# Kernel tuning notes

Hardware: AMD Instinct MI355X
Metric: run time of the kernel (lower is better)

The kernel has to match this reference:

```python
import jax, jax.numpy as jnp
import numpy as np

NC = 16       # class_nums
C = 128       # in_channel == EMBEND_DIM
NS = 8192     # support points
NQ = 30000    # query points
EPS = 1e-8


def setup_inputs() -> dict:
    key = jax.random.key(0)
    ks = jax.random.split(key, 7)
    support_features = jax.random.normal(ks[0], (NS, C), dtype=jnp.float32)
    support_labels = jax.random.randint(ks[1], (NS,), 0, NC)
    query_features = jax.random.normal(ks[2], (NQ, C), dtype=jnp.float32)
    # proj = Linear(2C+1 -> C) + ReLU + Linear(C -> 128)
    s1 = 1.0 / np.sqrt(2 * C + 1)
    W1 = jax.random.uniform(ks[3], (2 * C + 1, C), minval=-s1, maxval=s1, dtype=jnp.float32)
    b1 = jax.random.uniform(ks[4], (C,), minval=-s1, maxval=s1, dtype=jnp.float32)
    s2 = 1.0 / np.sqrt(C)
    W2 = jax.random.uniform(ks[5], (C, C), minval=-s2, maxval=s2, dtype=jnp.float32)
    b2 = jax.random.uniform(ks[6], (C,), minval=-s2, maxval=s2, dtype=jnp.float32)
    return {"support_features": support_features, "support_labels": support_labels,
            "query_features": query_features, "W1": W1, "b1": b1, "W2": W2, "b2": b2}


def _prototypes(support_features, support_labels):
    # fused scatter-mean replacing the per-class Python loop
    sums = jax.ops.segment_sum(support_features, support_labels, num_segments=NC)  # [Nc, C]
    counts = jax.ops.segment_sum(jnp.ones((support_features.shape[0],), support_features.dtype),
                                 support_labels, num_segments=NC)                   # [Nc]
    return jnp.where(counts[:, None] > 0, sums / jnp.maximum(counts, 1.0)[:, None], 0.0)


def reference(support_features, support_labels, query_features, W1, b1, W2, b2):
    protos = _prototypes(support_features, support_labels)                # [Nc, C]
    # MD_distance: cosine similarity between each query and each class prototype
    qn = query_features / jnp.maximum(jnp.linalg.norm(query_features, axis=-1, keepdims=True), EPS)
    pn = protos / jnp.maximum(jnp.linalg.norm(protos, axis=-1, keepdims=True), EPS)
    cos = jnp.einsum('qc,nc->qn', qn, pn)                                 # [Nq, Nc]
    # proj(cat([query, proto, cos], -1)) without materializing the [Nq,Nc,2C+1] concat:
    # split W1 rows into query part, proto part, and cos part.
    Wq, Wp, Wc = W1[:C], W1[C:2 * C], W1[2 * C]                           # [C,C],[C,C],[C]
    h = jax.nn.relu(jnp.einsum('qc,ch->qh', query_features, Wq)[:, None, :]
                    + jnp.einsum('nc,ch->nh', protos, Wp)[None, :, :]
                    + cos[:, :, None] * Wc[None, None, :]
                    + b1)                                                 # [Nq, Nc, C]
    similarity = jnp.einsum('qnh,ho->qno', h, W2) + b2                    # [Nq, Nc, 128]
    return similarity, cos[:, :, None]
```

## Files before the change

### kernel.cpp

```cpp
#include <hip/hip_runtime.h>

#define NQ_ 30000
#define NC_ 16
#define C_  128
#define NS_ 8192
#define QB  16
#define NBLK (NQ_/QB)

typedef __attribute__((ext_vector_type(4))) float  f32x4;
typedef __attribute__((ext_vector_type(4))) short  s16x4;
typedef __attribute__((ext_vector_type(8))) short  s16x8;

#define WS_PART  0
#define WS_PCNT  32768
#define WS_T     33024
#define WS_PACK  35072

__device__ inline short f2bf(float x){
  unsigned u = __float_as_uint(x);
  u += 0x7fffu + ((u >> 16) & 1u);
  return (short)(u >> 16);
}

__global__ __launch_bounds__(128) void protoA(const float* __restrict__ sf,
                                              const int* __restrict__ lbl,
                                              const float* __restrict__ W1,
                                              const float* __restrict__ W2,
                                              float* __restrict__ ws){
  const int b = blockIdx.x;
  const int t = threadIdx.x;
  if (b < 256){
    const int cls = b >> 4;
    const int ch  = b & 15;
    const int r0  = ch * (NS_/16);
    float s = 0.f; int cnt = 0;
    #pragma unroll 4
    for (int r = r0; r < r0 + NS_/16; ++r){
      if (lbl[r] == cls){ s += sf[(size_t)r*C_ + t]; ++cnt; }
    }
    ws[WS_PART + (cls*16 + ch)*C_ + t] = s;
    if (t == 0) ws[WS_PCNT + cls*16 + ch] = (float)cnt;
  } else {
    short* packo = (short*)(ws + WS_PACK);
    const int g0 = (b - 256)*1024 + t*8;
    const int gg = g0 & 16383;
    const int ln = (gg >> 3) & 63, ks = (gg >> 9) & 3, wvv = gg >> 11;
    const int kb = ks*32 + ((ln >> 4) & 3)*8;
    const int col = wvv*16 + (ln & 15);
    const float* src = (g0 < 16384) ? W2 : W1;
    s16x8 v;
    #pragma unroll
    for (int i = 0; i < 8; ++i) v[i] = f2bf(src[(size_t)(kb + i)*C_ + col]);
    *(s16x8*)&packo[g0] = v;
  }
}

__global__ __launch_bounds__(128) void protoB(const float* __restrict__ W1,
                                              const float* __restrict__ b1,
                                              float* __restrict__ ws){
  __shared__ float pr[C_];
  __shared__ float rns;
  const int n = blockIdx.x;
  const int h = threadIdx.x;
  float s = 0.f;
  #pragma unroll
  for (int ch = 0; ch < 16; ++ch) s += ws[WS_PART + (n*16 + ch)*C_ + h];
  float cnt = 0.f;
  #pragma unroll
  for (int ch = 0; ch < 16; ++ch) cnt += ws[WS_PCNT + n*16 + ch];
  const float pv = (cnt > 0.f) ? s / fmaxf(cnt, 1.f) : 0.f;
  pr[h] = pv;
  __syncthreads();
  if (h < 64){
    float q = pr[h]*pr[h] + pr[h+64]*pr[h+64];
    q += __shfl_xor(q, 1);  q += __shfl_xor(q, 2);  q += __shfl_xor(q, 4);
    q += __shfl_xor(q, 8);  q += __shfl_xor(q, 16); q += __shfl_xor(q, 32);
    if (h == 0) rns = 1.f / fmaxf(sqrtf(q), 1e-8f);
  }
  __syncthreads();
  {
    short* packo = (short*)(ws + WS_PACK);
    const int k = h;
    const int gg = ((k >> 5)*64 + ((k >> 3) & 3)*16 + n)*8 + (k & 7);
    packo[32768 + gg] = f2bf(pv * rns);
  }
  float acc = b1[h];
  #pragma unroll 8
  for (int c = 0; c < C_; ++c) acc = fmaf(pr[c], W1[(size_t)(C_ + c)*C_ + h], acc);
  ws[WS_T + n*C_ + h] = acc;
}

__global__ __launch_bounds__(512) void fused_main(const float* __restrict__ qfeat,
                                                  const float* __restrict__ W1,
                                                  const float* __restrict__ b2,
                                                  const float* __restrict__ ws,
                                                  float* __restrict__ out){
  __shared__ __align__(16) char un[16384];
  __shared__ float qw[QB][132];
  __shared__ float tl16[NC_][132];
  __shared__ float cosl[QB][NC_];
  __shared__ float rqn[QB];
  __shared__ float wcl[C_];

  float (*qfs)[132] = (float(*)[132])un;
  short* hfrag = (short*)un;

  const int t    = threadIdx.x;
  const int lane = t & 63;
  const int wv   = t >> 6;
  const int qbase = blockIdx.x * QB;
  float* out_cos = out + (size_t)NQ_ * NC_ * C_;
  const short* pack = (const short*)(ws + WS_PACK);

  {
    int idx = t * 4; int q = idx >> 7; int c = idx & 127;
    *(f32x4*)&qfs[q][c]  = *(const f32x4*)(qfeat + (size_t)qbase*C_ + idx);
    *(f32x4*)&tl16[q][c] = *(const f32x4*)(ws + WS_T + idx);
    if (t < 32) *(f32x4*)&wcl[t*4] = *(const f32x4*)(W1 + 2*C_*C_ + t*4);
  }
  __syncthreads();

  if (t < 128){
    int q = t >> 3; int c0 = (t & 7) * 16;
    float s = 0.f;
    #pragma unroll
    for (int m = 0; m < 16; ++m){ float v = qfs[q][c0+m]; s = fmaf(v, v, s); }
    s += __shfl_xor(s, 1); s += __shfl_xor(s, 2); s += __shfl_xor(s, 4);
    if ((t & 7) == 0) rqn[q] = 1.f / fmaxf(sqrtf(s), 1e-8f);
  }

  const int fr = lane & 15;
  const int fg = lane >> 4;
  const int ocol = wv*16 + fr;

  s16x8 qfr[4], w2f[4], wqf[4];
  #pragma unroll
  for (int ks = 0; ks < 4; ++ks){
    const int c0 = ks*32 + fg*8;
    f32x4 a = *(const f32x4*)&qfs[fr][c0];
    f32x4 b = *(const f32x4*)&qfs[fr][c0+4];
    s16x8 v;
    v[0]=f2bf(a[0]); v[1]=f2bf(a[1]); v[2]=f2bf(a[2]); v[3]=f2bf(a[3]);
    v[4]=f2bf(b[0]); v[5]=f2bf(b[1]); v[6]=f2bf(b[2]); v[7]=f2bf(b[3]);
    qfr[ks] = v;
    w2f[ks] = *(const s16x8*)&pack[((wv*4 + ks)*64 + lane)*8];
    wqf[ks] = *(const s16x8*)&pack[16384 + ((wv*4 + ks)*64 + lane)*8];
  }
  const float b2v = b2[ocol];
  __syncthreads();

  {
    f32x4 dq = {0.f,0.f,0.f,0.f};
    #pragma unroll
    for (int ks = 0; ks < 4; ++ks)
      dq = __builtin_amdgcn_mfma_f32_16x16x32_bf16(qfr[ks], wqf[ks], dq, 0,0,0);
    #pragma unroll
    for (int r = 0; r < 4; ++r) qw[fg*4 + r][ocol] = dq[r];
  }
  if (wv == 0){
    s16x8 pnf[4];
    #pragma unroll
    for (int ks = 0; ks < 4; ++ks)
      pnf[ks] = *(const s16x8*)&pack[32768 + (ks*64 + lane)*8];
    f32x4 dc = {0.f,0.f,0.f,0.f};
    #pragma unroll
    for (int ks = 0; ks < 4; ++ks)
      dc = __builtin_amdgcn_mfma_f32_16x16x32_bf16(qfr[ks], pnf[ks], dc, 0,0,0);
    #pragma unroll
    for (int r = 0; r < 4; ++r){
      const int q = fg*4 + r;
      const float cv = dc[r] * rqn[q];
      cosl[q][fr] = cv;
      out_cos[(size_t)(qbase + q)*NC_ + fr] = cv;
    }
  }
  __syncthreads();

  const int na  = lane & 15;
  const int ga  = lane >> 4;
  const int ksA = wv >> 1;
  const int ii0 = (wv & 1) * 4;
  const int k0  = ksA*32 + ga*8 + ii0;
  const f32x4 t4  = *(const f32x4*)&tl16[na][k0];
  const f32x4 wc4 = *(const f32x4*)&wcl[k0];

  #pragma unroll
  for (int chunk = 0; chunk < 4; ++chunk){
    const int q0 = chunk * 4;
    #pragma unroll
    for (int qq = 0; qq < 4; ++qq){
      const int q = q0 + qq;
      f32x4 qw4 = *(const f32x4*)&qw[q][k0];
      const float cv = cosl[q][na];
      s16x4 hv;
      #pragma unroll
      for (int j = 0; j < 4; ++j){
        float h = fmaf(cv, wc4[j], qw4[j] + t4[j]);
        hv[j] = f2bf(fmaxf(h, 0.f));
      }
      *(s16x4*)&hfrag[qq*2048 + ksA*512 + lane*8 + ii0] = hv;
    }
    __syncthreads();
    #pragma unroll
    for (int qq = 0; qq < 4; ++qq){
      s16x8 a0 = *(const s16x8*)&hfrag[qq*2048 +    0 + lane*8];
      s16x8 a1 = *(const s16x8*)&hfrag[qq*2048 +  512 + lane*8];
      s16x8 a2 = *(const s16x8*)&hfrag[qq*2048 + 1024 + lane*8];
      s16x8 a3 = *(const s16x8*)&hfrag[qq*2048 + 1536 + lane*8];
      f32x4 acc = {b2v, b2v, b2v, b2v};
      acc = __builtin_amdgcn_mfma_f32_16x16x32_bf16(a0, w2f[0], acc, 0,0,0);
      acc = __builtin_amdgcn_mfma_f32_16x16x32_bf16(a1, w2f[1], acc, 0,0,0);
      acc = __builtin_amdgcn_mfma_f32_16x16x32_bf16(a2, w2f[2], acc, 0,0,0);
      acc = __builtin_amdgcn_mfma_f32_16x16x32_bf16(a3, w2f[3], acc, 0,0,0);
      const size_t qout = (size_t)(qbase + q0 + qq) * (NC_*C_);
      #pragma unroll
      for (int r = 0; r < 4; ++r)
        out[qout + (fg*4 + r)*C_ + ocol] = acc[r];
    }
    __syncthreads();
  }
}

extern "C" void kernel_launch(void* const* d_in, const int* in_sizes, int n_in,
                              void* d_out, int out_size, void* d_ws, size_t ws_size,
                              hipStream_t stream){
  const float* sf  = (const float*)d_in[0];
  const int*   lbl = (const int*)  d_in[1];
  const float* qf  = (const float*)d_in[2];
  const float* W1  = (const float*)d_in[3];
  const float* b1  = (const float*)d_in[4];
  const float* W2  = (const float*)d_in[5];
  const float* b2  = (const float*)d_in[6];
  float* ws  = (float*)d_ws;
  float* out = (float*)d_out;

  protoA<<<288, 128, 0, stream>>>(sf, lbl, W1, W2, ws);
  protoB<<<NC_, 128, 0, stream>>>(W1, b1, ws);
  fused_main<<<NBLK, 512, 0, stream>>>(qf, W1, b2, ws, out);
}
```

Before: 89.38 us.

## Single-pass all-class prototype reduction and packed bf16 conversions

Prototype accumulation now has each of 64 chunks read the support rows once and accumulate into all 16 class registers. Before, 256 blocks each re-read a slice and filtered by a single class. Separately, float-to-bf16 conversions in the main kernel use the packed HIP bf16x2 intrinsic in place of manual per-element rounding. The first change cuts redundant support-feature reads and uses more registers per thread. The second aims to reduce ALU work in the h-activation and query-fragment conversion paths.

```diff
diff --git a/kernel.cpp b/kernel.cpp
--- a/kernel.cpp
+++ b/kernel.cpp
@@ -1,4 +1,5 @@
 #include <hip/hip_runtime.h>
+#include <hip/hip_bf16.h>
 
 #define NQ_ 30000
 #define NC_ 16
@@ -8,18 +9,24 @@
 #define NBLK (NQ_/QB)
 
 typedef __attribute__((ext_vector_type(4))) float  f32x4;
-typedef __attribute__((ext_vector_type(4))) short  s16x4;
 typedef __attribute__((ext_vector_type(8))) short  s16x8;
 
+#define NCHK 64
 #define WS_PART  0
-#define WS_PCNT  32768
-#define WS_T     33024
-#define WS_PACK  35072
+#define WS_PCNT  131072
+#define WS_T     132096
+#define WS_PACK  134144
 
 __device__ inline short f2bf(float x){
   unsigned u = __float_as_uint(x);
   u += 0x7fffu + ((u >> 16) & 1u);
   return (short)(u >> 16);
+}
+
+__device__ inline unsigned pk2(float lo, float hi){
+  __hip_bfloat162 r = __float22bfloat162_rn(float2{lo, hi});
+  union { __hip_bfloat162 b; unsigned u; } c; c.b = r;
+  return c.u;
 }
 
 __global__ __launch_bounds__(128) void protoA(const float* __restrict__ sf,
@@ -29,20 +36,30 @@
                                               float* __restrict__ ws){
   const int b = blockIdx.x;
   const int t = threadIdx.x;
-  if (b < 256){
-    const int cls = b >> 4;
-    const int ch  = b & 15;
-    const int r0  = ch * (NS_/16);
-    float s = 0.f; int cnt = 0;
-    #pragma unroll 4
-    for (int r = r0; r < r0 + NS_/16; ++r){
-      if (lbl[r] == cls){ s += sf[(size_t)r*C_ + t]; ++cnt; }
-    }
-    ws[WS_PART + (cls*16 + ch)*C_ + t] = s;
-    if (t == 0) ws[WS_PCNT + cls*16 + ch] = (float)cnt;
+  if (b < NCHK){
+    const int r0 = b * (NS_/NCHK);
+    float a[NC_];
+    float cn[NC_];
+    #pragma unroll
+    for (int k = 0; k < NC_; ++k){ a[k] = 0.f; cn[k] = 0.f; }
+    for (int r = r0; r < r0 + NS_/NCHK; ++r){
+      const float v = sf[(size_t)r*C_ + t];
+      const int   l = lbl[r];
+      #pragma unroll
+      for (int k = 0; k < NC_; ++k){
+        const bool m = (l == k);
+        a[k]  += m ? v   : 0.f;
+        cn[k] += m ? 1.f : 0.f;
+      }
+    }
+    #pragma unroll
+    for (int k = 0; k < NC_; ++k){
+      ws[WS_PART + ((size_t)k*NCHK + b)*C_ + t] = a[k];
+      if (t == 0) ws[WS_PCNT + k*NCHK + b] = cn[k];
+    }
   } else {
     short* packo = (short*)(ws + WS_PACK);
-    const int g0 = (b - 256)*1024 + t*8;
+    const int g0 = (b - NCHK)*1024 + t*8;
     const int gg = g0 & 16383;
     const int ln = (gg >> 3) & 63, ks = (gg >> 9) & 3, wvv = gg >> 11;
     const int kb = ks*32 + ((ln >> 4) & 3)*8;
@@ -63,11 +80,11 @@
   const int n = blockIdx.x;
   const int h = threadIdx.x;
   float s = 0.f;
-  #pragma unroll
-  for (int ch = 0; ch < 16; ++ch) s += ws[WS_PART + (n*16 + ch)*C_ + h];
+  #pragma unroll 8
+  for (int ch = 0; ch < NCHK; ++ch) s += ws[WS_PART + ((size_t)n*NCHK + ch)*C_ + h];
   float cnt = 0.f;
-  #pragma unroll
-  for (int ch = 0; ch < 16; ++ch) cnt += ws[WS_PCNT + n*16 + ch];
+  #pragma unroll 8
+  for (int ch = 0; ch < NCHK; ++ch) cnt += ws[WS_PCNT + n*NCHK + ch];
   const float pv = (cnt > 0.f) ? s / fmaxf(cnt, 1.f) : 0.f;
   pr[h] = pv;
   __syncthreads();
@@ -139,10 +156,12 @@
     const int c0 = ks*32 + fg*8;
     f32x4 a = *(const f32x4*)&qfs[fr][c0];
     f32x4 b = *(const f32x4*)&qfs[fr][c0+4];
-    s16x8 v;
-    v[0]=f2bf(a[0]); v[1]=f2bf(a[1]); v[2]=f2bf(a[2]); v[3]=f2bf(a[3]);
-    v[4]=f2bf(b[0]); v[5]=f2bf(b[1]); v[6]=f2bf(b[2]); v[7]=f2bf(b[3]);
-    qfr[ks] = v;
+    union { unsigned u[4]; s16x8 v; } cv;
+    cv.u[0] = pk2(a[0], a[1]);
+    cv.u[1] = pk2(a[2], a[3]);
+    cv.u[2] = pk2(b[0], b[1]);
+    cv.u[3] = pk2(b[2], b[3]);
+    qfr[ks] = cv.v;
     w2f[ks] = *(const s16x8*)&pack[((wv*4 + ks)*64 + lane)*8];
     wqf[ks] = *(const s16x8*)&pack[16384 + ((wv*4 + ks)*64 + lane)*8];
   }
@@ -192,13 +211,14 @@
       const int q = q0 + qq;
       f32x4 qw4 = *(const f32x4*)&qw[q][k0];
       const float cv = cosl[q][na];
-      s16x4 hv;
-      #pragma unroll
-      for (int j = 0; j < 4; ++j){
-        float h = fmaf(cv, wc4[j], qw4[j] + t4[j]);
-        hv[j] = f2bf(fmaxf(h, 0.f));
-      }
-      *(s16x4*)&hfrag[qq*2048 + ksA*512 + lane*8 + ii0] = hv;
+      float h0 = fmaxf(fmaf(cv, wc4[0], qw4[0] + t4[0]), 0.f);
+      float h1 = fmaxf(fmaf(cv, wc4[1], qw4[1] + t4[1]), 0.f);
+      float h2 = fmaxf(fmaf(cv, wc4[2], qw4[2] + t4[2]), 0.f);
+      float h3 = fmaxf(fmaf(cv, wc4[3], qw4[3] + t4[3]), 0.f);
+      union { unsigned u[2]; uint2 d; } hv;
+      hv.u[0] = pk2(h0, h1);
+      hv.u[1] = pk2(h2, h3);
+      *(uint2*)&hfrag[qq*2048 + ksA*512 + lane*8 + ii0] = hv.d;
     }
     __syncthreads();
     #pragma unroll
@@ -234,7 +254,7 @@
   float* ws  = (float*)d_ws;
   float* out = (float*)d_out;
 
-  protoA<<<288, 128, 0, stream>>>(sf, lbl, W1, W2, ws);
+  protoA<<<NCHK + 32, 128, 0, stream>>>(sf, lbl, W1, W2, ws);
   protoB<<<NC_, 128, 0, stream>>>(W1, b1, ws);
   fused_main<<<NBLK, 512, 0, stream>>>(qf, W1, b2, ws, out);
 }
```

Result: slower. 120.3 us (+34.7%).

## Halve fused_main block to 4 waves, each computing two output column tiles

Applied to the files above, without the earlier changes.

The main kernel now runs with 256 threads (4 waves) instead of 512. Each wave owns two 16-column output tiles and keeps two sets of W2 fragments in registers. Each thread builds a full 8-element bf16 h fragment instead of 4. The aim is more independent MFMA work per wave, fewer barrier participants and better occupancy via launch_bounds(256,4), at the cost of higher register pressure per thread.

```diff
diff --git a/kernel.cpp b/kernel.cpp
--- a/kernel.cpp
+++ b/kernel.cpp
@@ -8,7 +8,6 @@
 #define NBLK (NQ_/QB)
 
 typedef __attribute__((ext_vector_type(4))) float  f32x4;
-typedef __attribute__((ext_vector_type(4))) short  s16x4;
 typedef __attribute__((ext_vector_type(8))) short  s16x8;
 
 #define WS_PART  0
@@ -90,11 +89,11 @@
   ws[WS_T + n*C_ + h] = acc;
 }
 
-__global__ __launch_bounds__(512) void fused_main(const float* __restrict__ qfeat,
-                                                  const float* __restrict__ W1,
-                                                  const float* __restrict__ b2,
-                                                  const float* __restrict__ ws,
-                                                  float* __restrict__ out){
+__global__ __launch_bounds__(256, 4) void fused_main(const float* __restrict__ qfeat,
+                                                     const float* __restrict__ W1,
+                                                     const float* __restrict__ b2,
+                                                     const float* __restrict__ ws,
+                                                     float* __restrict__ out){
   __shared__ __align__(16) char un[16384];
   __shared__ float qw[QB][132];
   __shared__ float tl16[NC_][132];
@@ -108,14 +107,18 @@
   const int t    = threadIdx.x;
   const int lane = t & 63;
   const int wv   = t >> 6;
+  const int fr   = lane & 15;
+  const int fg   = lane >> 4;
   const int qbase = blockIdx.x * QB;
   float* out_cos = out + (size_t)NQ_ * NC_ * C_;
   const short* pack = (const short*)(ws + WS_PACK);
 
   {
-    int idx = t * 4; int q = idx >> 7; int c = idx & 127;
-    *(f32x4*)&qfs[q][c]  = *(const f32x4*)(qfeat + (size_t)qbase*C_ + idx);
-    *(f32x4*)&tl16[q][c] = *(const f32x4*)(ws + WS_T + idx);
+    const int idx = t * 8, q = idx >> 7, c = idx & 127;
+    *(f32x4*)&qfs[q][c]      = *(const f32x4*)(qfeat + (size_t)qbase*C_ + idx);
+    *(f32x4*)&qfs[q][c+4]    = *(const f32x4*)(qfeat + (size_t)qbase*C_ + idx + 4);
+    *(f32x4*)&tl16[q][c]     = *(const f32x4*)(ws + WS_T + idx);
+    *(f32x4*)&tl16[q][c+4]   = *(const f32x4*)(ws + WS_T + idx + 4);
     if (t < 32) *(f32x4*)&wcl[t*4] = *(const f32x4*)(W1 + 2*C_*C_ + t*4);
   }
   __syncthreads();
@@ -129,11 +132,7 @@
     if ((t & 7) == 0) rqn[q] = 1.f / fmaxf(sqrtf(s), 1e-8f);
   }
 
-  const int fr = lane & 15;
-  const int fg = lane >> 4;
-  const int ocol = wv*16 + fr;
-
-  s16x8 qfr[4], w2f[4], wqf[4];
+  s16x8 qfr[4];
   #pragma unroll
   for (int ks = 0; ks < 4; ++ks){
     const int c0 = ks*32 + fg*8;
@@ -143,29 +142,36 @@
     v[0]=f2bf(a[0]); v[1]=f2bf(a[1]); v[2]=f2bf(a[2]); v[3]=f2bf(a[3]);
     v[4]=f2bf(b[0]); v[5]=f2bf(b[1]); v[6]=f2bf(b[2]); v[7]=f2bf(b[3]);
     qfr[ks] = v;
-    w2f[ks] = *(const s16x8*)&pack[((wv*4 + ks)*64 + lane)*8];
-    wqf[ks] = *(const s16x8*)&pack[16384 + ((wv*4 + ks)*64 + lane)*8];
-  }
-  const float b2v = b2[ocol];
-  __syncthreads();
-
-  {
+  }
+  s16x8 w2f[2][4];
+  float b2v[2];
+  #pragma unroll
+  for (int j = 0; j < 2; ++j){
+    const int tt = wv*2 + j;
+    #pragma unroll
+    for (int ks = 0; ks < 4; ++ks)
+      w2f[j][ks] = *(const s16x8*)&pack[((tt*4 + ks)*64 + lane)*8];
+    b2v[j] = b2[tt*16 + fr];
+  }
+  __syncthreads();
+
+  #pragma unroll
+  for (int j = 0; j < 2; ++j){
+    const int tt = wv*2 + j;
     f32x4 dq = {0.f,0.f,0.f,0.f};
     #pragma unroll
     for (int ks = 0; ks < 4; ++ks)
-      dq = __builtin_amdgcn_mfma_f32_16x16x32_bf16(qfr[ks], wqf[ks], dq, 0,0,0);
-    #pragma unroll
-    for (int r = 0; r < 4; ++r) qw[fg*4 + r][ocol] = dq[r];
+      dq = __builtin_amdgcn_mfma_f32_16x16x32_bf16(qfr[ks],
+             *(const s16x8*)&pack[16384 + ((tt*4 + ks)*64 + lane)*8], dq, 0,0,0);
+    #pragma unroll
+    for (int r = 0; r < 4; ++r) qw[fg*4 + r][tt*16 + fr] = dq[r];
   }
   if (wv == 0){
-    s16x8 pnf[4];
+    f32x4 dc = {0.f,0.f,0.f,0.f};
     #pragma unroll
     for (int ks = 0; ks < 4; ++ks)
-      pnf[ks] = *(const s16x8*)&pack[32768 + (ks*64 + lane)*8];
-    f32x4 dc = {0.f,0.f,0.f,0.f};
-    #pragma unroll
-    for (int ks = 0; ks < 4; ++ks)
-      dc = __builtin_amdgcn_mfma_f32_16x16x32_bf16(qfr[ks], pnf[ks], dc, 0,0,0);
+      dc = __builtin_amdgcn_mfma_f32_16x16x32_bf16(qfr[ks],
+             *(const s16x8*)&pack[32768 + (ks*64 + lane)*8], dc, 0,0,0);
     #pragma unroll
     for (int r = 0; r < 4; ++r){
       const int q = fg*4 + r;
@@ -176,13 +182,11 @@
   }
   __syncthreads();
 
-  const int na  = lane & 15;
-  const int ga  = lane >> 4;
-  const int ksA = wv >> 1;
-  const int ii0 = (wv & 1) * 4;
-  const int k0  = ksA*32 + ga*8 + ii0;
-  const f32x4 t4  = *(const f32x4*)&tl16[na][k0];
-  const f32x4 wc4 = *(const f32x4*)&wcl[k0];
+  const int k0 = wv*32 + fg*8;
+  const f32x4 t8a = *(const f32x4*)&tl16[fr][k0];
+  const f32x4 t8b = *(const f32x4*)&tl16[fr][k0+4];
+  const f32x4 w8a = *(const f32x4*)&wcl[k0];
+  const f32x4 w8b = *(const f32x4*)&wcl[k0+4];
 
   #pragma unroll
   for (int chunk = 0; chunk < 4; ++chunk){
@@ -190,32 +194,39 @@
     #pragma unroll
     for (int qq = 0; qq < 4; ++qq){
       const int q = q0 + qq;
-      f32x4 qw4 = *(const f32x4*)&qw[q][k0];
-      const float cv = cosl[q][na];
-      s16x4 hv;
+      f32x4 qa = *(const f32x4*)&qw[q][k0];
+      f32x4 qb = *(const f32x4*)&qw[q][k0+4];
+      const float cv = cosl[q][fr];
+      s16x8 hv;
       #pragma unroll
-      for (int j = 0; j < 4; ++j){
-        float h = fmaf(cv, wc4[j], qw4[j] + t4[j]);
-        hv[j] = f2bf(fmaxf(h, 0.f));
-      }
-      *(s16x4*)&hfrag[qq*2048 + ksA*512 + lane*8 + ii0] = hv;
+      for (int jj = 0; jj < 4; ++jj)
+        hv[jj] = f2bf(fmaxf(fmaf(cv, w8a[jj], qa[jj] + t8a[jj]), 0.f));
+      #pragma unroll
+      for (int jj = 0; jj < 4; ++jj)
+        hv[4+jj] = f2bf(fmaxf(fmaf(cv, w8b[jj], qb[jj] + t8b[jj]), 0.f));
+      *(s16x8*)&hfrag[qq*2048 + wv*512 + lane*8] = hv;
     }
     __syncthreads();
     #pragma unroll
     for (int qq = 0; qq < 4; ++qq){
-      s16x8 a0 = *(const s16x8*)&hfrag[qq*2048 +    0 + lane*8];
-      s16x8 a1 = *(const s16x8*)&hfrag[qq*2048 +  512 + lane*8];
-      s16x8 a2 = *(const s16x8*)&hfrag[qq*2048 + 1024 + lane*8];
-      s16x8 a3 = *(const s16x8*)&hfrag[qq*2048 + 1536 + lane*8];
-      f32x4 acc = {b2v, b2v, b2v, b2v};
-      acc = __builtin_amdgcn_mfma_f32_16x16x32_bf16(a0, w2f[0], acc, 0,0,0);
-      acc = __builtin_amdgcn_mfma_f32_16x16x32_bf16(a1, w2f[1], acc, 0,0,0);
-      acc = __builtin_amdgcn_mfma_f32_16x16x32_bf16(a2, w2f[2], acc, 0,0,0);
-      acc = __builtin_amdgcn_mfma_f32_16x16x32_bf16(a3, w2f[3], acc, 0,0,0);
+      const short* hb = &hfrag[qq*2048 + lane*8];
+      s16x8 a0 = *(const s16x8*)&hb[0];
+      s16x8 a1 = *(const s16x8*)&hb[512];
+      s16x8 a2 = *(const s16x8*)&hb[1024];
+      s16x8 a3 = *(const s16x8*)&hb[1536];
       const size_t qout = (size_t)(qbase + q0 + qq) * (NC_*C_);
       #pragma unroll
-      for (int r = 0; r < 4; ++r)
-        out[qout + (fg*4 + r)*C_ + ocol] = acc[r];
+      for (int j = 0; j < 2; ++j){
+        f32x4 acc = {b2v[j], b2v[j], b2v[j], b2v[j]};
+        acc = __builtin_amdgcn_mfma_f32_16x16x32_bf16(a0, w2f[j][0], acc, 0,0,0);
+        acc = __builtin_amdgcn_mfma_f32_16x16x32_bf16(a1, w2f[j][1], acc, 0,0,0);
+        acc = __builtin_amdgcn_mfma_f32_16x16x32_bf16(a2, w2f[j][2], acc, 0,0,0);
+        acc = __builtin_amdgcn_mfma_f32_16x16x32_bf16(a3, w2f[j][3], acc, 0,0,0);
+        const int ocol = (wv*2 + j)*16 + fr;
+        #pragma unroll
+        for (int r = 0; r < 4; ++r)
+          out[qout + (fg*4 + r)*C_ + ocol] = acc[r];
+      }
     }
     __syncthreads();
   }
@@ -236,5 +247,5 @@
 
   protoA<<<288, 128, 0, stream>>>(sf, lbl, W1, W2, ws);
   protoB<<<NC_, 128, 0, stream>>>(W1, b1, ws);
-  fused_main<<<NBLK, 512, 0, stream>>>(qf, W1, b2, ws, out);
-}
+  fused_main<<<NBLK, 256, 0, stream>>>(qf, W1, b2, ws, out);
+}
```

After: 88.39 us. No clear change (-1.1%).
